# Kernel optimization log

Hardware: AMD Instinct MI355X
Metric: run time of the kernel (lower is better)

## Reference

```python
import jax, jax.numpy as jnp
import numpy as np

B, N, C, D = 2, 6, 64, 40
FH, FW = 12, 33
IMG_H, IMG_W = 384, 1056
NX, NY, NZ = 100, 100, 4
LOWER = np.array([-50.0, -50.0, -10.0], np.float32)   # xbound[0], ybound[0], zbound[0]
DXV = np.array([1.0, 1.0, 5.0], np.float32)           # voxel sizes


def _conv(x, w, pad):
    return jax.lax.conv_general_dilated(x, w, (1, 1), [(pad, pad), (pad, pad)],
                                        dimension_numbers=('NCHW', 'OIHW', 'NCHW'))


def _bn(x, s, b):
    return x * s[None, :, None, None] + b[None, :, None, None]


def _se(x, w1, b1, w2, b2):
    m = x.mean((2, 3))                                   # global avg pool -> (B, C)
    g = jax.nn.sigmoid(jax.nn.silu(m @ w1.T + b1) @ w2.T + b2)
    return x * g[:, :, None, None]


def _frustum():
    ds = jnp.arange(4.0, 44.0, 1.0)                      # (D,) depth bins
    xs = jnp.linspace(0.0, IMG_W - 1.0, FW)
    ys = jnp.linspace(0.0, IMG_H - 1.0, FH)
    f = jnp.stack(jnp.broadcast_arrays(xs[None, None, :], ys[None, :, None], ds[:, None, None]), -1)
    return f.reshape(-1, 3)                              # (D*FH*FW, 3) in (x_px, y_px, depth)


def reference(feats, rots, trans, intrinsics, nw1, bn1s, bn1b, se1w1, se1b1, se1w2, se1b2,
              nw2, bn2s, bn2b, dhw, dhb, chw, chb, bcw1, bcs1, bcb1, bcsw1, bcsb1, bcsw2,
              bcsb2, bcw2, bcs2, bcb2, dw1, ds1, db1, dw2, db2):
    BN = B * N
    # ---- CamEncoderV2 neck + heads (backbone 1280ch@1/32 features given directly) ----
    x = jax.nn.silu(_bn(_conv(feats, nw1, 0), bn1s, bn1b))
    x = _se(x, se1w1, se1b1, se1w2, se1b2)
    x = jax.nn.silu(_bn(_conv(x, nw2, 1), bn2s, bn2b))
    depth = jax.nn.softmax(_conv(x, dhw, 0) + dhb[None, :, None, None], axis=1)  # (BN, D, FH, FW)
    ctx = _conv(x, chw, 0) + chb[None, :, None, None]                            # (BN, C, FH, FW)
    # ---- geometry: pixel frustum -> ego-frame points ----
    rots_f = rots.reshape(BN, 3, 3)
    trans_f = trans.reshape(BN, 3)
    K = intrinsics.reshape(BN, 3, 3)
    pts = _frustum()                                     # (P0, 3), P0 = D*FH*FW
    d = pts[:, 2]
    fx, fy = K[:, 0, 0][:, None], K[:, 1, 1][:, None]
    cx, cy = K[:, 0, 2][:, None], K[:, 1, 2][:, None]
    cam = jnp.stack([(pts[None, :, 0] - cx) * d[None, :] / fx,
                     (pts[None, :, 1] - cy) * d[None, :] / fy,
                     jnp.broadcast_to(d[None, :], (BN, d.shape[0]))], -1)        # (BN, P0, 3)
    geom = jnp.einsum('bij,bpj->bpi', rots_f, cam) + trans_f[:, None, :]
    geom = geom.reshape(B, -1, 3)                        # (B, N*P0, 3)
    # ---- lift: outer product context x depth ----
    ff = (ctx[:, None, :, :, :] * depth[:, :, None, :, :])                       # (BN, D, C, FH, FW)
    ff = ff.transpose(0, 1, 3, 4, 2).reshape(B, -1, C)                           # (B, N*P0, C)
    # ---- splat: voxel pooling (scatter-add into BEV grid) ----
    idx = jnp.floor((geom - jnp.asarray(LOWER)) / jnp.asarray(DXV)).astype(jnp.int32)
    valid = jnp.all((idx >= 0) & (idx < jnp.array([NX, NY, NZ])), axis=-1)
    sid = idx[..., 2] * (NX * NY) + idx[..., 0] * NY + idx[..., 1]
    sid = jnp.where(valid, sid, 0)
    ffm = ff * valid[..., None]
    pooled = jax.vmap(lambda f, i: jax.ops.segment_sum(f, i, num_segments=NZ * NX * NY))(ffm, sid)
    bev = pooled.reshape(B, NZ, NX, NY, C).transpose(0, 1, 4, 2, 3).reshape(B, NZ * C, NX, NY)
    # ---- BEVCompressorV2 (residual conv-SE-conv) ----
    h = jax.nn.relu(_bn(_conv(bev, bcw1, 1), bcs1, bcb1))
    h = _se(h, bcsw1, bcsb1, bcsw2, bcsb2)
    h = jax.nn.relu(_bn(_conv(h, bcw2, 1), bcs2, bcb2))
    bev = bev + h
    # ---- decoder ----
    h = jax.nn.relu(_bn(_conv(bev, dw1, 1), ds1, db1))
    out = _conv(h, dw2, 0) + db2[None, :, None, None]    # (B, nz*num_classes, NX, NY)
    return out.reshape(B, 4, NZ, NX, NY)


def setup_inputs():
    f32 = jnp.float32
    ks = jax.random.split(jax.random.key(0), 16)
    feats = jax.random.normal(ks[0], (B * N, 1280, FH, FW), f32) * 0.5
    # cam->ego: z_cam -> x_ego, -x_cam -> y_ego, -y_cam -> z_ego, plus per-camera yaw
    Rbase = np.array([[0., 0., 1.], [-1., 0., 0.], [0., -1., 0.]], np.float32)
    yaw = np.deg2rad(np.arange(N) * 60.0).astype(np.float32)
    c, s = np.cos(yaw), np.sin(yaw)
    Rz = np.zeros((N, 3, 3), np.float32)
    Rz[:, 0, 0] = c; Rz[:, 0, 1] = -s; Rz[:, 1, 0] = s; Rz[:, 1, 1] = c; Rz[:, 2, 2] = 1.0
    rots = jnp.asarray(np.broadcast_to(np.einsum('nij,jk->nik', Rz, Rbase), (B, N, 3, 3)).copy())
    trans = jax.random.normal(ks[1], (B, N, 3), f32) * 1.0
    K = np.array([[800., 0., 528.], [0., 800., 192.], [0., 0., 1.]], np.float32)
    intrinsics = jnp.asarray(np.broadcast_to(K, (B, N, 3, 3)).copy())

    def w(k, shape, fan_in):
        return jax.random.normal(k, shape, f32) * np.float32(np.sqrt(2.0 / fan_in))

    kk = jax.random.split(ks[2], 16)
    return dict(
        feats=feats, rots=rots, trans=trans, intrinsics=intrinsics,
        nw1=w(kk[0], (256, 1280, 1, 1), 1280), bn1s=jnp.ones(256, f32), bn1b=jnp.zeros(256, f32),
        se1w1=w(kk[1], (32, 256), 256), se1b1=jnp.zeros(32, f32),
        se1w2=w(kk[2], (256, 32), 32), se1b2=jnp.zeros(256, f32),
        nw2=w(kk[3], (256, 256, 3, 3), 2304), bn2s=jnp.ones(256, f32), bn2b=jnp.zeros(256, f32),
        dhw=w(kk[4], (40, 256, 1, 1), 256), dhb=jnp.zeros(40, f32),
        chw=w(kk[5], (64, 256, 1, 1), 256), chb=jnp.zeros(64, f32),
        bcw1=w(kk[6], (256, 256, 3, 3), 2304), bcs1=jnp.ones(256, f32), bcb1=jnp.zeros(256, f32),
        bcsw1=w(kk[7], (16, 256), 256), bcsb1=jnp.zeros(16, f32),
        bcsw2=w(kk[8], (256, 16), 16), bcsb2=jnp.zeros(256, f32),
        bcw2=w(kk[9], (256, 256, 3, 3), 2304), bcs2=jnp.ones(256, f32), bcb2=jnp.zeros(256, f32),
        dw1=w(kk[10], (128, 256, 3, 3), 2304), ds1=jnp.ones(128, f32), db1=jnp.zeros(128, f32),
        dw2=w(kk[11], (16, 128, 1, 1), 128), db2=jnp.zeros(16, f32),
    )
```

## Files before the change

### kernel.cpp

```cpp
#include <hip/hip_runtime.h>
#include <hip/hip_bf16.h>
#include <cmath>


typedef __attribute__((ext_vector_type(8))) short short8;
typedef __attribute__((ext_vector_type(4))) float floatx4;
typedef __hip_bfloat16 hb;

__device__ __forceinline__ float sigf(float x){ return 1.0f/(1.0f+expf(-x)); }
__device__ __forceinline__ float siluf(float x){ return x*sigf(x); }
__device__ __forceinline__ void split2(float v, hb* h, hb* l){
  hb hv = __float2bfloat16(v);
  *h = hv; *l = __float2bfloat16(v - __bfloat162float(hv));
}

__global__ __launch_bounds__(256) void k_trans_featsP(
    const float* __restrict__ feats, hb* __restrict__ Fph, hb* __restrict__ Fpl)
{
  __shared__ float tile[64][65];
  int n = blockIdx.z;
  int p0 = blockIdx.x*64;
  int c0 = blockIdx.y*64;
  int tid = threadIdx.x;
  int tr = tid >> 6;
  int tc = tid & 63;
  #pragma unroll
  for (int it=0; it<16; ++it){
    int ci = c0 + it*4 + tr;
    int p = p0 + tc;
    float v = 0.f;
    if (p < 396) v = feats[((size_t)n*1280 + ci)*396 + p];
    tile[it*4+tr][tc] = v;
  }
  __syncthreads();
  #pragma unroll
  for (int iter=0; iter<2; ++iter){
    int idx = iter*256 + tid;
    int oc = idx >> 6;
    int pl = idx & 63;
    int p = p0 + pl;
    if (p < 396){
      int P = n*396 + p;
      int T = P >> 4, mm = P & 15;
      int kb = (c0 >> 5) + (oc >> 2);
      int q = oc & 3;
      int lane = q*16 + mm;
      size_t o = (((size_t)T*40 + kb)*64 + lane)*8;
      #pragma unroll
      for (int j=0; j<8; ++j){
        hb hv, lv; split2(tile[oc*8+j][pl], &hv, &lv);
        Fph[o+j] = hv; Fpl[o+j] = lv;
      }
    }
  }
}

__global__ __launch_bounds__(256) void k_wpack1(
    const float* __restrict__ W, hb* __restrict__ Wph, hb* __restrict__ Wpl)
{
  int i = blockIdx.x*256 + threadIdx.x;
  if (i >= 40*16*512) return;
  int j = i & 7;
  int lane = (i>>3) & 63;
  int t2 = i >> 9;
  int nb = t2 & 15;
  int kb = t2 >> 4;
  int ci = kb*32 + (lane>>4)*8 + j;
  int co = nb*16 + (lane&15);
  hb hv, lv; split2(W[(size_t)co*1280 + ci], &hv, &lv);
  Wph[i] = hv; Wpl[i] = lv;
}

__global__ __launch_bounds__(256) void k_wpack(
    const float* __restrict__ W, hb* __restrict__ Wph, hb* __restrict__ Wpl, int NB)
{
  int i = blockIdx.x*256 + threadIdx.x;
  int total = 9*8*NB*512;
  if (i >= total) return;
  int j = i & 7;
  int t1 = i >> 3;
  int lane = t1 & 63;
  int t2 = t1 >> 6;
  int nb = t2 % NB;
  int t3 = t2 / NB;
  int kb = t3 & 7;
  int tap = t3 >> 3;
  int ci = kb*32 + (lane>>4)*8 + j;
  int co = nb*16 + (lane&15);
  hb hv, lv; split2(W[(size_t)co*2304 + ci*9 + tap], &hv, &lv);
  Wph[i] = hv; Wpl[i] = lv;
}

__global__ __launch_bounds__(256) void k_wpackT(
    const float* __restrict__ W, hb* __restrict__ Wph, hb* __restrict__ Wpl, int NB)
{
  int i = blockIdx.x*256 + threadIdx.x;
  int total = 9*8*NB*512;
  if (i >= total) return;
  int j = i & 7;
  int t1 = i >> 3;
  int lane = t1 & 63;
  int t2 = t1 >> 6;
  int nb = t2 % NB;
  int t3 = t2 / NB;
  int tap = t3 % 9;
  int kb = t3 / 9;
  int ci = kb*32 + (lane>>4)*8 + j;
  int co = nb*16 + (lane&15);
  hb hv, lv; split2(W[(size_t)co*2304 + ci*9 + tap], &hv, &lv);
  Wph[i] = hv; Wpl[i] = lv;
}

__global__ __launch_bounds__(256) void k_wpackH(
    const float* __restrict__ dhw, const float* __restrict__ chw,
    hb* __restrict__ Wph, hb* __restrict__ Wpl)
{
  int i = blockIdx.x*256 + threadIdx.x;
  if (i >= 8*7*512) return;
  int j = i & 7;
  int t1 = i >> 3;
  int lane = t1 & 63;
  int t2 = t1 >> 6;
  int nb = t2 % 7;
  int kb = t2 / 7;
  int ci = kb*32 + (lane>>4)*8 + j;
  int co = nb*16 + (lane&15);
  float w = 0.f;
  if (co < 40) w = dhw[(size_t)co*256 + ci];
  else if (co < 104) w = chw[(size_t)(co-40)*256 + ci];
  hb hv, lv; split2(w, &hv, &lv);
  Wph[i] = hv; Wpl[i] = lv;
}

__global__ __launch_bounds__(256) void k_mfma_gemm1(
    const hb* __restrict__ Fph, const hb* __restrict__ Fpl,
    const hb* __restrict__ Wph, const hb* __restrict__ Wpl,
    const float* __restrict__ bns, const float* __restrict__ bnb,
    float* __restrict__ out)
{
  __shared__ short8 lbh[256], lbl[256];
  int tid = threadIdx.x;
  int wv = tid >> 6, lane = tid & 63;
  int cog = blockIdx.y;
  int Pbase = blockIdx.x*128 + wv*32;
  int q = lane >> 4;
  int T0 = blockIdx.x*8 + wv*2; if (T0 > 296) T0 = 296;
  int T1 = T0 + 1;              if (T1 > 296) T1 = 296;
  size_t a0 = (size_t)T0*2560 + lane;
  size_t a1 = (size_t)T1*2560 + lane;
  const short8* gAh = (const short8*)(const void*)Fph;
  const short8* gAl = (const short8*)(const void*)Fpl;
  const short8* gWh = (const short8*)(const void*)Wph;
  const short8* gWl = (const short8*)(const void*)Wpl;
  size_t sb = (size_t)(cog*4 + wv)*64 + lane;
  floatx4 acc[2][4];
  #pragma unroll
  for (int i=0;i<2;++i)
    #pragma unroll
    for (int j=0;j<4;++j) acc[i][j] = (floatx4)(0.f);
  short8 ph = gWh[sb], pw = gWl[sb];
  short8 cah0 = gAh[a0], cal0 = gAl[a0], cah1 = gAh[a1], cal1 = gAl[a1];
  for (int kb=0; kb<40; ++kb){
    __syncthreads();
    lbh[tid] = ph; lbl[tid] = pw;
    int nx = (kb+1 < 40) ? kb+1 : 39;
    ph = gWh[(size_t)nx*1024 + sb]; pw = gWl[(size_t)nx*1024 + sb];
    __syncthreads();
    short8 nah0 = gAh[a0 + (size_t)nx*64];
    short8 nal0 = gAl[a0 + (size_t)nx*64];
    short8 nah1 = gAh[a1 + (size_t)nx*64];
    short8 nal1 = gAl[a1 + (size_t)nx*64];
    #pragma unroll
    for (int nb=0; nb<4; ++nb){
      short8 bh = lbh[nb*64 + lane];
      short8 bl = lbl[nb*64 + lane];
      acc[0][nb] = __builtin_amdgcn_mfma_f32_16x16x32_bf16(cah0, bh, acc[0][nb], 0,0,0);
      acc[0][nb] = __builtin_amdgcn_mfma_f32_16x16x32_bf16(cah0, bl, acc[0][nb], 0,0,0);
      acc[0][nb] = __builtin_amdgcn_mfma_f32_16x16x32_bf16(cal0, bh, acc[0][nb], 0,0,0);
      acc[1][nb] = __builtin_amdgcn_mfma_f32_16x16x32_bf16(cah1, bh, acc[1][nb], 0,0,0);
      acc[1][nb] = __builtin_amdgcn_mfma_f32_16x16x32_bf16(cah1, bl, acc[1][nb], 0,0,0);
      acc[1][nb] = __builtin_amdgcn_mfma_f32_16x16x32_bf16(cal1, bh, acc[1][nb], 0,0,0);
    }
    cah0 = nah0; cal0 = nal0; cah1 = nah1; cal1 = nal1;
  }
  int n16 = lane & 15;
  #pragma unroll
  for (int mg=0; mg<2; ++mg){
    #pragma unroll
    for (int nb=0; nb<4; ++nb){
      int co = cog*64 + nb*16 + n16;
      float s = bns[co], bv = bnb[co];
      #pragma unroll
      for (int r=0; r<4; ++r){
        int P = Pbase + mg*16 + q*4 + r;
        if (P < 4752) out[(size_t)P*256 + co] = siluf(acc[mg][nb][r]*s + bv);
      }
    }
  }
}

__global__ __launch_bounds__(256) void k_meanN(
    const float* __restrict__ x1, float* __restrict__ mean)
{
  int n = blockIdx.x; int c = threadIdx.x;
  float s = 0.f;
  for (int p=0; p<396; ++p) s += x1[((size_t)n*396+p)*256 + c];
  mean[n*256+c] = s*(1.f/396.f);
}

__global__ __launch_bounds__(256) void k_se_fc(
    const float* __restrict__ mean, const float* __restrict__ w1, const float* __restrict__ b1,
    const float* __restrict__ w2, const float* __restrict__ b2, float* __restrict__ g,
    int H, float inv)
{
  __shared__ float m[256];
  __shared__ float h[32];
  int n = blockIdx.x; int t = threadIdx.x;
  m[t] = mean[n*256 + t] * inv;
  __syncthreads();
  if (t < H){
    float s = b1[t];
    for (int c=0; c<256; ++c) s += m[c]*w1[t*256+c];
    h[t] = siluf(s);
  }
  __syncthreads();
  float s = b2[t];
  for (int j=0; j<H; ++j) s += h[j]*w2[t*H+j];
  g[n*256+t] = sigf(s);
}

__global__ __launch_bounds__(256) void k_topad(
    const float* __restrict__ x1, const float* __restrict__ g,
    hb* __restrict__ Xh, hb* __restrict__ Xl)
{
  int y = blockIdx.x;
  int n = blockIdx.y;
  int c = threadIdx.x;
  float gc = g[n*256+c];
  for (int xx=0; xx<35; ++xx){
    float v = 0.f;
    if (y>=1 && y<=12 && xx>=1 && xx<=33)
      v = x1[((size_t)n*396 + (y-1)*33 + (xx-1))*256 + c]*gc;
    hb hv, lv; split2(v, &hv, &lv);
    size_t o = (((size_t)n*14+y)*35+xx)*256 + c;
    Xh[o] = hv; Xl[o] = lv;
  }
}

__global__ __launch_bounds__(256) void k_conv3s_mfma(
    const hb* __restrict__ Xh, const hb* __restrict__ Xl,
    const hb* __restrict__ Wph, const hb* __restrict__ Wpl,
    const float* __restrict__ bns, const float* __restrict__ bnb,
    hb* __restrict__ outh, hb* __restrict__ outl)
{
  __shared__ short8 lbh[256], lbl[256];
  int tid = threadIdx.x;
  int wv = tid >> 6, lane = tid & 63;
  int cog = blockIdx.y;
  int Pbase = blockIdx.x*128 + wv*32;
  int m = lane & 15, q = lane >> 4;
  int P0 = Pbase + m;      if (P0 > 4751) P0 = 4751;
  int P1 = Pbase + 16 + m; if (P1 > 4751) P1 = 4751;
  int n0 = P0/396, pim0 = P0%396;
  int n1 = P1/396, pim1 = P1%396;
  size_t base0 = (size_t)((n0*14 + pim0/33)*35 + pim0%33)*32 + q;
  size_t base1 = (size_t)((n1*14 + pim1/33)*35 + pim1%33)*32 + q;
  const short8* gAh = (const short8*)(const void*)Xh;
  const short8* gAl = (const short8*)(const void*)Xl;
  const short8* gWh = (const short8*)(const void*)Wph;
  const short8* gWl = (const short8*)(const void*)Wpl;
  size_t sb = (size_t)(cog*4 + wv)*64 + lane;
  floatx4 acc[2][4];
  #pragma unroll
  for (int i=0;i<2;++i)
    #pragma unroll
    for (int j=0;j<4;++j) acc[i][j] = (floatx4)(0.f);
  short8 ph = gWh[sb], pw = gWl[sb];
  short8 cah0 = gAh[base0], cal0 = gAl[base0], cah1 = gAh[base1], cal1 = gAl[base1];
  for (int idx=0; idx<72; ++idx){
    __syncthreads();
    lbh[tid] = ph; lbl[tid] = pw;
    int nx = (idx+1 < 72) ? idx+1 : 71;
    ph = gWh[(size_t)nx*1024 + sb]; pw = gWl[(size_t)nx*1024 + sb];
    __syncthreads();
    int tap = nx >> 3, kb = nx & 7;
    int dy = (tap*11) >> 5;
    int dx = tap - dy*3;
    int ao = (dy*35+dx)*32 + kb*4;
    short8 nah0 = gAh[base0 + ao];
    short8 nal0 = gAl[base0 + ao];
    short8 nah1 = gAh[base1 + ao];
    short8 nal1 = gAl[base1 + ao];
    #pragma unroll
    for (int nb=0; nb<4; ++nb){
      short8 bh = lbh[nb*64 + lane];
      short8 bl = lbl[nb*64 + lane];
      acc[0][nb] = __builtin_amdgcn_mfma_f32_16x16x32_bf16(cah0, bh, acc[0][nb], 0,0,0);
      acc[0][nb] = __builtin_amdgcn_mfma_f32_16x16x32_bf16(cah0, bl, acc[0][nb], 0,0,0);
      acc[0][nb] = __builtin_amdgcn_mfma_f32_16x16x32_bf16(cal0, bh, acc[0][nb], 0,0,0);
      acc[1][nb] = __builtin_amdgcn_mfma_f32_16x16x32_bf16(cah1, bh, acc[1][nb], 0,0,0);
      acc[1][nb] = __builtin_amdgcn_mfma_f32_16x16x32_bf16(cah1, bl, acc[1][nb], 0,0,0);
      acc[1][nb] = __builtin_amdgcn_mfma_f32_16x16x32_bf16(cal1, bh, acc[1][nb], 0,0,0);
    }
    cah0 = nah0; cal0 = nal0; cah1 = nah1; cal1 = nal1;
  }
  int n16 = lane & 15;
  #pragma unroll
  for (int mg=0; mg<2; ++mg){
    #pragma unroll
    for (int r=0; r<4; ++r){
      int P = Pbase + mg*16 + q*4 + r;
      if (P < 4752){
        #pragma unroll
        for (int nb=0; nb<4; ++nb){
          int co = cog*64 + nb*16 + n16;
          float v = siluf(acc[mg][nb][r]*bns[co] + bnb[co]);
          hb hv, lv; split2(v, &hv, &lv);
          outh[(size_t)P*256 + co] = hv;
          outl[(size_t)P*256 + co] = lv;
        }
      }
    }
  }
}

__global__ __launch_bounds__(256) void k_headsM(
    const hb* __restrict__ x2h, const hb* __restrict__ x2l,
    const hb* __restrict__ Whh, const hb* __restrict__ Whl,
    const float* __restrict__ dhb, const float* __restrict__ chb,
    float* __restrict__ dep, float* __restrict__ ctx2)
{
  __shared__ short8 lbh[256], lbl[256];
  int tid = threadIdx.x;
  int wv = tid >> 6, lane = tid & 63;
  int cog = blockIdx.y;
  int nb0 = cog*4;
  int nbN = cog ? 3 : 4;
  int Pbase = blockIdx.x*128 + wv*32;
  int m = lane & 15, q = lane >> 4;
  int P0 = Pbase + m;      if (P0 > 4751) P0 = 4751;
  int P1 = Pbase + 16 + m; if (P1 > 4751) P1 = 4751;
  size_t rA0 = (size_t)P0*32 + q;
  size_t rA1 = (size_t)P1*32 + q;
  const short8* gAh = (const short8*)(const void*)x2h;
  const short8* gAl = (const short8*)(const void*)x2l;
  const short8* gWh = (const short8*)(const void*)Whh;
  const short8* gWl = (const short8*)(const void*)Whl;
  floatx4 acc[2][4];
  #pragma unroll
  for (int i=0;i<2;++i)
    #pragma unroll
    for (int j=0;j<4;++j) acc[i][j] = (floatx4)(0.f);
  for (int kb=0; kb<8; ++kb){
    __syncthreads();
    for (int i=tid; i<nbN*64; i+=256){
      lbh[i] = gWh[(size_t)(kb*7 + nb0)*64 + i];
      lbl[i] = gWl[(size_t)(kb*7 + nb0)*64 + i];
    }
    __syncthreads();
    short8 ah0 = gAh[rA0 + kb*4], al0 = gAl[rA0 + kb*4];
    short8 ah1 = gAh[rA1 + kb*4], al1 = gAl[rA1 + kb*4];
    for (int nb=0; nb<nbN; ++nb){
      short8 bh = lbh[nb*64 + lane];
      short8 bl = lbl[nb*64 + lane];
      acc[0][nb] = __builtin_amdgcn_mfma_f32_16x16x32_bf16(ah0, bh, acc[0][nb], 0,0,0);
      acc[0][nb] = __builtin_amdgcn_mfma_f32_16x16x32_bf16(ah0, bl, acc[0][nb], 0,0,0);
      acc[0][nb] = __builtin_amdgcn_mfma_f32_16x16x32_bf16(al0, bh, acc[0][nb], 0,0,0);
      acc[1][nb] = __builtin_amdgcn_mfma_f32_16x16x32_bf16(ah1, bh, acc[1][nb], 0,0,0);
      acc[1][nb] = __builtin_amdgcn_mfma_f32_16x16x32_bf16(ah1, bl, acc[1][nb], 0,0,0);
      acc[1][nb] = __builtin_amdgcn_mfma_f32_16x16x32_bf16(al1, bh, acc[1][nb], 0,0,0);
    }
  }
  int n16 = lane & 15;
  #pragma unroll
  for (int mg=0; mg<2; ++mg){
    #pragma unroll
    for (int r=0; r<4; ++r){
      int P = Pbase + mg*16 + q*4 + r;
      if (P < 4752){
        int nn = P/396, pim = P%396;
        for (int nb=0; nb<nbN; ++nb){
          int co = cog*64 + nb*16 + n16;
          float v = acc[mg][nb][r];
          if (co < 40)
            dep[((size_t)nn*40 + co)*396 + pim] = v + dhb[co];
          else if (co < 104)
            ctx2[((size_t)nn*396 + pim)*64 + (co-40)] = v + chb[co-40];
        }
      }
    }
  }
}

__global__ __launch_bounds__(256) void k_softmax40(float* __restrict__ dep)
{
  int i = blockIdx.x*256 + threadIdx.x;
  if (i >= 12*396) return;
  int n = i/396, p = i%396;
  float* base = dep + (size_t)n*40*396 + p;
  float mx = -1e30f;
  for (int d=0; d<40; ++d) mx = fmaxf(mx, base[(size_t)d*396]);
  float s = 0.f;
  for (int d=0; d<40; ++d){ float e = expf(base[(size_t)d*396]-mx); base[(size_t)d*396]=e; s+=e; }
  float inv = 1.f/s;
  for (int d=0; d<40; ++d) base[(size_t)d*396] *= inv;
}

__global__ __launch_bounds__(256) void k_geom(
    const float* __restrict__ rots, const float* __restrict__ trans,
    const float* __restrict__ intr, int* __restrict__ vox, int* __restrict__ cnt)
{
  int pt = blockIdx.x*256 + threadIdx.x;
  if (pt >= 190080) return;
  int b = pt/95040; int r = pt%95040;
  int n = r/15840;  int r2 = r%15840;
  int d = r2/396;   int pim = r2%396;
  int y = pim/33, x = pim%33;
  int bn = b*6+n;
  const float* R = rots + (size_t)bn*9;
  const float* T = trans + (size_t)bn*3;
  const float* K = intr + (size_t)bn*9;
  float fx=K[0], cx=K[2], fy=K[4], cy=K[5];
  float xs = (float)x * 32.96875f;
  float ys = (float)((double)y * (383.0/11.0));
  float dv = 4.0f + (float)d;
  float camx = (xs-cx)*dv/fx;
  float camy = (ys-cy)*dv/fy;
  float gx = R[0]*camx + R[1]*camy + R[2]*dv + T[0];
  float gy = R[3]*camx + R[4]*camy + R[5]*dv + T[1];
  float gz = R[6]*camx + R[7]*camy + R[8]*dv + T[2];
  int ix = (int)floorf(gx + 50.f);
  int iy = (int)floorf(gy + 50.f);
  int iz = (int)floorf((gz + 10.f)/5.f);
  bool valid = (ix>=0 && ix<100 && iy>=0 && iy<100 && iz>=0 && iz<4);
  int sid = iz*10000 + ix*100 + iy;
  vox[pt] = valid ? sid : -1;
  if (valid) atomicAdd(&cnt[b*40000 + sid], 1);
}

__global__ __launch_bounds__(256) void k_scan1(
    const int* __restrict__ cnt, int* __restrict__ off, int* __restrict__ bsum)
{
  __shared__ int s[256];
  int t = threadIdx.x;
  int i = blockIdx.x*256 + t;
  int v = (i < 80000) ? cnt[i] : 0;
  s[t] = v; __syncthreads();
  for (int o=1;o<256;o<<=1){
    int x = (t>=o) ? s[t-o] : 0;
    __syncthreads();
    s[t] += x;
    __syncthreads();
  }
  if (i < 80000) off[i] = s[t] - v;
  if (t == 255) bsum[blockIdx.x] = s[255];
}

__global__ void k_scan2(int* __restrict__ bsum, int nblk)
{
  if (threadIdx.x==0 && blockIdx.x==0){
    int run = 0;
    for (int j=0;j<nblk;++j){ int t = bsum[j]; bsum[j] = run; run += t; }
  }
}

__global__ __launch_bounds__(256) void k_scan3(
    int* __restrict__ off, const int* __restrict__ bsum, int* __restrict__ cur)
{
  int i = blockIdx.x*256 + threadIdx.x;
  if (i >= 80000) return;
  int o = off[i] + bsum[i>>8];
  off[i] = o;
  cur[i] = o;
}

__global__ __launch_bounds__(256) void k_fill(
    const int* __restrict__ vox, int* __restrict__ cur, int* __restrict__ list)
{
  int pt = blockIdx.x*256 + threadIdx.x;
  if (pt >= 190080) return;
  int s = vox[pt];
  if (s < 0) return;
  int b = pt/95040;
  int slot = atomicAdd(&cur[b*40000 + s], 1);
  list[slot] = pt;
}

__global__ __launch_bounds__(256) void k_gather(
    const int* __restrict__ off, const int* __restrict__ cnt, const int* __restrict__ list,
    const float* __restrict__ ctx2, const float* __restrict__ dep, float* __restrict__ bev)
{
  int tid = threadIdx.x;
  int bv = blockIdx.x*4 + (tid>>6);
  int c = tid & 63;
  int b = bv/40000, sid = bv%40000;
  int st = off[bv], nn = cnt[bv];
  float s = 0.f;
  for (int k=0;k<nn;++k){
    int pt = list[st+k];
    int r = pt%95040;
    int bn = b*6 + r/15840;
    int r2 = r%15840;
    int dd = r2/396, pim = r2%396;
    s += ctx2[((size_t)bn*396+pim)*64 + c] * dep[((size_t)bn*40+dd)*396 + pim];
  }
  int iz = sid/10000, rem = sid%10000;
  bev[(size_t)b*2560000 + (size_t)iz*640000 + (size_t)c*10000 + rem] = s;
}

__global__ __launch_bounds__(256) void k_tohwc2(
    const float* __restrict__ in, hb* __restrict__ Ah, hb* __restrict__ Al,
    const float* __restrict__ g)
{
  __shared__ float tile[32*105];
  int py = blockIdx.x;
  int b  = blockIdx.y;
  int cg = blockIdx.z;
  int tid = threadIdx.x;
  bool inner = (py >= 1 && py <= 100);
  if (inner){
    if (tid < 64){ int cil = tid & 31; int col = (tid>>5) ? 101 : 0; tile[cil*105 + col] = 0.f; }
    for (int i = tid; i < 3200; i += 256){
      int cil = i / 100, x = i % 100;
      int ci = cg*32 + cil;
      tile[cil*105 + (x+1)] = in[(((size_t)b*256 + ci)*100 + (py-1))*100 + x];
    }
  }
  __syncthreads();
  for (int i = tid; i < 32*102; i += 256){
    int px = i >> 5, cil = i & 31;
    int ci = cg*32 + cil;
    float v = 0.f;
    if (inner){
      v = tile[cil*105 + px];
      if (g) v *= g[b*256 + ci];
    }
    hb hv, lv; split2(v, &hv, &lv);
    size_t o = (((size_t)b*102 + py)*102 + px)*256 + ci;
    Ah[o] = hv; Al[o] = lv;
  }
}

__global__ __launch_bounds__(256) void k_rowmean(
    const float* __restrict__ in, float* __restrict__ out, int rowlen, float inv)
{
  __shared__ float ws[4];
  int row = blockIdx.x; int t = threadIdx.x;
  const float* p = in + (size_t)row*rowlen;
  float s = 0.f;
  for (int i=t; i<rowlen; i+=256) s += p[i];
  #pragma unroll
  for (int off=32; off; off>>=1) s += __shfl_down(s, off);
  if ((t&63)==0) ws[t>>6] = s;
  __syncthreads();
  if (t==0) out[row] = (ws[0]+ws[1]+ws[2]+ws[3]) * inv;
}

__global__ __launch_bounds__(256) void k_conv3_bevm(
    const hb* __restrict__ Ah, const hb* __restrict__ Al,
    const hb* __restrict__ Wph, const hb* __restrict__ Wpl,
    const float* __restrict__ bns, const float* __restrict__ bnb,
    const float* __restrict__ res, float* __restrict__ out, int Cout, int NBG)
{
  __shared__ __align__(16) short sAh[10*18*44];
  __shared__ __align__(16) short sAl[10*18*44];
  __shared__ short8 lbh[2][256], lbl[2][256];
  const int NB = Cout >> 4;
  int tid = threadIdx.x;
  int wv = tid >> 6, lane = tid & 63;
  int L = blockIdx.x;
  int spatial = L / (NBG*2);
  int rem = L % (NBG*2);
  int cog = rem % NBG;
  int bb  = rem / NBG;
  int xg = spatial % 7, yg = spatial / 7;
  int x0 = xg*16;
  int y0 = yg*8 + wv;
  int m = lane & 15, q = lane >> 4;
  int nb0 = cog*4;
  floatx4 acc[2][4];
  #pragma unroll
  for (int i=0;i<2;++i)
    #pragma unroll
    for (int j=0;j<4;++j) acc[i][j] = (floatx4)(0.f);

  const short8* gAh = (const short8*)(const void*)Ah;
  const short8* gAl = (const short8*)(const void*)Al;
  const short8* gWh = (const short8*)(const void*)Wph;
  const short8* gWl = (const short8*)(const void*)Wpl;
  const size_t nbstride = (size_t)NB*64;
  const size_t sb = (size_t)(nb0 + wv)*64 + lane;

  short8 ph = gWh[sb], pl = gWl[sb];
  int cur = 0;

  for (int kb=0; kb<8; ++kb){
    #pragma unroll 3
    for (int tap=0; tap<9; ++tap){
      int idx2 = kb*9 + tap;
      if (tap == 0){
        __syncthreads();
        for (int i = tid; i < 720; i += 256){
          int rc = i >> 2, part = i & 3;
          int r = rc / 18, c = rc % 18;
          int yr = yg*8 + r; if (yr > 101) yr = 101;
          int xc = x0 + c;   if (xc > 101) xc = 101;
          size_t so = ((size_t)((bb*102 + yr)*102 + xc))*32 + kb*4 + part;
          short8 vh = gAh[so], vl = gAl[so];
          int dst = (r*18 + c)*44 + part*8;
          *(short8*)(sAh + dst) = vh;
          *(short8*)(sAl + dst) = vl;
        }
      }
      lbh[cur][tid] = ph; lbl[cur][tid] = pl;
      int nx = (idx2+1 < 72) ? idx2+1 : 71;
      ph = gWh[(size_t)nx*nbstride + sb];
      pl = gWl[(size_t)nx*nbstride + sb];
      __syncthreads();
      int dy = (tap*11) >> 5;
      int dx = tap - dy*3;
      int cc = dx + m;
      int a0 = ((wv + dy)*18 + cc)*44 + q*8;
      int a1 = ((wv + 4 + dy)*18 + cc)*44 + q*8;
      short8 cah0 = *(const short8*)(sAh + a0);
      short8 cal0 = *(const short8*)(sAl + a0);
      short8 cah1 = *(const short8*)(sAh + a1);
      short8 cal1 = *(const short8*)(sAl + a1);
      #pragma unroll
      for (int nb=0; nb<4; ++nb){
        short8 bh = lbh[cur][nb*64 + lane];
        short8 bl = lbl[cur][nb*64 + lane];
        acc[0][nb] = __builtin_amdgcn_mfma_f32_16x16x32_bf16(cah0, bh, acc[0][nb], 0,0,0);
        acc[0][nb] = __builtin_amdgcn_mfma_f32_16x16x32_bf16(cah0, bl, acc[0][nb], 0,0,0);
        acc[0][nb] = __builtin_amdgcn_mfma_f32_16x16x32_bf16(cal0, bh, acc[0][nb], 0,0,0);
        acc[1][nb] = __builtin_amdgcn_mfma_f32_16x16x32_bf16(cah1, bh, acc[1][nb], 0,0,0);
        acc[1][nb] = __builtin_amdgcn_mfma_f32_16x16x32_bf16(cah1, bl, acc[1][nb], 0,0,0);
        acc[1][nb] = __builtin_amdgcn_mfma_f32_16x16x32_bf16(cal1, bh, acc[1][nb], 0,0,0);
      }
      cur ^= 1;
    }
  }

  int n = lane & 15;
  int xq = x0 + q*4;
  #pragma unroll
  for (int mg=0; mg<2; ++mg){
    int yo = y0 + mg*4;
    if (yo < 100 && xq < 100){
      #pragma unroll
      for (int nb=0; nb<4; ++nb){
        int co = cog*64 + nb*16 + n;
        float s = bns[co], bv = bnb[co];
        floatx4 a = acc[mg][nb];
        float4 v;
        v.x = fmaxf(a[0]*s+bv, 0.f);
        v.y = fmaxf(a[1]*s+bv, 0.f);
        v.z = fmaxf(a[2]*s+bv, 0.f);
        v.w = fmaxf(a[3]*s+bv, 0.f);
        size_t o = ((size_t)(bb*Cout+co)*100 + yo)*100 + xq;
        if (res){
          float4 rv = *(const float4*)(res + o);
          v.x += rv.x; v.y += rv.y; v.z += rv.z; v.w += rv.w;
        }
        *(float4*)(out + o) = v;
      }
    }
  }
}

__global__ __launch_bounds__(256) void k_final2(
    const float* __restrict__ h, const float* __restrict__ W, const float* __restrict__ bias,
    float* __restrict__ out)
{
  __shared__ float wsl[2048];
  __shared__ float bs[16];
  int tid = threadIdx.x;
  int b = blockIdx.y;
  for (int i=tid; i<2048; i+=256) wsl[i] = W[i];
  if (tid < 16) bs[tid] = bias[tid];
  __syncthreads();
  int pix = blockIdx.x*256 + tid;
  if (pix >= 10000) return;
  float acc[16];
  #pragma unroll
  for (int oc=0; oc<16; ++oc) acc[oc] = bs[oc];
  const float* hb_ = h + (size_t)b*128*10000 + pix;
  for (int ci=0; ci<128; ++ci){
    float hv = hb_[(size_t)ci*10000];
    #pragma unroll
    for (int oc=0; oc<16; ++oc) acc[oc] += hv * wsl[oc*128 + ci];
  }
  #pragma unroll
  for (int oc=0; oc<16; ++oc)
    out[((size_t)(b*16+oc))*10000 + pix] = acc[oc];
}

extern "C" void kernel_launch(void* const* d_in, const int* in_sizes, int n_in,
                              void* d_out, int out_size, void* d_ws, size_t ws_size,
                              hipStream_t stream)
{
  (void)in_sizes; (void)n_in; (void)out_size; (void)ws_size;
  const float* feats = (const float*)d_in[0];
  const float* rots  = (const float*)d_in[1];
  const float* trans = (const float*)d_in[2];
  const float* intr  = (const float*)d_in[3];
  const float* nw1   = (const float*)d_in[4];
  const float* bn1s  = (const float*)d_in[5];
  const float* bn1b  = (const float*)d_in[6];
  const float* se1w1 = (const float*)d_in[7];
  const float* se1b1 = (const float*)d_in[8];
  const float* se1w2 = (const float*)d_in[9];
  const float* se1b2 = (const float*)d_in[10];
  const float* nw2   = (const float*)d_in[11];
  const float* bn2s  = (const float*)d_in[12];
  const float* bn2b  = (const float*)d_in[13];
  const float* dhw   = (const float*)d_in[14];
  const float* dhb   = (const float*)d_in[15];
  const float* chw   = (const float*)d_in[16];
  const float* chb   = (const float*)d_in[17];
  const float* bcw1  = (const float*)d_in[18];
  const float* bcs1  = (const float*)d_in[19];
  const float* bcb1  = (const float*)d_in[20];
  const float* bcsw1 = (const float*)d_in[21];
  const float* bcsb1 = (const float*)d_in[22];
  const float* bcsw2 = (const float*)d_in[23];
  const float* bcsb2 = (const float*)d_in[24];
  const float* bcw2  = (const float*)d_in[25];
  const float* bcs2  = (const float*)d_in[26];
  const float* bcb2  = (const float*)d_in[27];
  const float* dw1   = (const float*)d_in[28];
  const float* ds1   = (const float*)d_in[29];
  const float* db1   = (const float*)d_in[30];
  const float* dw2   = (const float*)d_in[31];
  const float* db2   = (const float*)d_in[32];
  float* out = (float*)d_out;

  float* ws = (float*)d_ws;
  float* bev   = ws;
  float* h1    = ws + 5120000;
  hb*    Ah    = (hb*)(ws + 10240000);
  hb*    Al    = (hb*)(ws + 12903424);
  float* x2    = ws + 15566848;
  float* S5    = ws + 16783360;
  float* dep   = ws + 17373184;
  float* ctx2  = ws + 17563264;
  float* mean1 = ws + 17867392;
  float* g1    = mean1 + 3072;
  float* mean2 = g1 + 3072;
  float* g2    = mean2 + 512;
  int*   vox   = (int*)(ws + 17875584);
  hb* Fph  = (hb*)bev;
  hb* Wc1h = (hb*)(bev + 3041280);
  hb* Wc1l = (hb*)(bev + 3205120);
  float* x1 = h1;
  hb* Fpl  = (hb*)(h1 + 1216512);
  hb* Xh   = (hb*)Ah;
  hb* Xl   = (hb*)Al;
  hb* Wc2h = (hb*)S5;
  hb* Wc2l = (hb*)(S5 + 294912);
  hb* x2h  = (hb*)x2;
  hb* x2l  = (hb*)(x2 + 608256);
  hb* Whh  = (hb*)S5;
  hb* Whl  = (hb*)(S5 + 14336);
  int* cnt  = (int*)h1;
  int* off  = cnt + 80000;
  int* cur  = off + 80000;
  int* bsum = cur + 80000;
  int* list = bsum + 1024;
  float* h3 = h1;
  hb* Wp1h = (hb*)x2;
  hb* Wp1l = (hb*)(x2 + 294912);
  hb* Wp3h = (hb*)(x2 + 589824);
  hb* Wp3l = (hb*)(x2 + 589824 + 147456);
  hb* Wp2h = (hb*)S5;
  hb* Wp2l = (hb*)(S5 + 294912);

  k_trans_featsP<<<dim3(7,20,12),256,0,stream>>>(feats,Fph,Fpl);
  k_wpack1<<<1280,256,0,stream>>>(nw1,Wc1h,Wc1l);
  k_mfma_gemm1<<<dim3(38,4),256,0,stream>>>(Fph,Fpl,Wc1h,Wc1l,bn1s,bn1b,x1);
  k_meanN<<<12,256,0,stream>>>(x1,mean1);
  k_se_fc<<<12,256,0,stream>>>(mean1,se1w1,se1b1,se1w2,se1b2,g1,32,1.f);
  k_topad<<<dim3(14,12),256,0,stream>>>(x1,g1,Xh,Xl);
  k_wpack<<<2304,256,0,stream>>>(nw2,Wc2h,Wc2l,16);
  k_conv3s_mfma<<<dim3(38,4),256,0,stream>>>(Xh,Xl,Wc2h,Wc2l,bn2s,bn2b,x2h,x2l);
  k_wpackH<<<112,256,0,stream>>>(dhw,chw,Whh,Whl);
  k_headsM<<<dim3(38,2),256,0,stream>>>(x2h,x2l,Whh,Whl,dhb,chb,dep,ctx2);
  k_softmax40<<<19,256,0,stream>>>(dep);

  k_wpackT<<<2304,256,0,stream>>>(bcw1,Wp1h,Wp1l,16);
  k_wpackT<<<2304,256,0,stream>>>(bcw2,Wp2h,Wp2l,16);
  k_wpackT<<<1152,256,0,stream>>>(dw1,Wp3h,Wp3l,8);

  hipMemsetAsync(cnt, 0, 80000*sizeof(int), stream);
  k_geom<<<(190080+255)/256,256,0,stream>>>(rots,trans,intr,vox,cnt);
  k_scan1<<<313,256,0,stream>>>(cnt,off,bsum);
  k_scan2<<<1,64,0,stream>>>(bsum,313);
  k_scan3<<<(80000+255)/256,256,0,stream>>>(off,bsum,cur);
  k_fill<<<(190080+255)/256,256,0,stream>>>(vox,cur,list);
  k_gather<<<20000,256,0,stream>>>(off,cnt,list,ctx2,dep,bev);

  k_tohwc2<<<dim3(102,2,8),256,0,stream>>>(bev,Ah,Al,nullptr);
  k_conv3_bevm<<<728,256,0,stream>>>(Ah,Al,Wp1h,Wp1l,bcs1,bcb1,nullptr,h1,256,4);
  k_rowmean<<<512,256,0,stream>>>(h1,mean2,10000,1e-4f);
  k_se_fc<<<2,256,0,stream>>>(mean2,bcsw1,bcsb1,bcsw2,bcsb2,g2,16,1.f);
  k_tohwc2<<<dim3(102,2,8),256,0,stream>>>(h1,Ah,Al,g2);
  k_conv3_bevm<<<728,256,0,stream>>>(Ah,Al,Wp2h,Wp2l,bcs2,bcb2,bev,bev,256,4);
  k_tohwc2<<<dim3(102,2,8),256,0,stream>>>(bev,Ah,Al,nullptr);
  k_conv3_bevm<<<364,256,0,stream>>>(Ah,Al,Wp3h,Wp3l,ds1,db1,nullptr,h3,128,2);
  k_final2<<<dim3(40,2),256,0,stream>>>(h3,dw2,db2,out);
}
```

Before: 687.0 us.

## Merge weight-pack and SE kernels, tile image conv in LDS, fuse BEV repack into gather

Several weight-packing launches are merged into two kernels, and the mean and SE-FC steps are fused into one kernel. The image 3x3 conv is rewritten to stage a spatial input tile in LDS per channel block and reuse it across the nine taps, with double-buffered weight fragments. The BEV gather now writes the padded bf16 hi/lo HWC layout directly, and a small kernel zeros the padding ring, so the first k_tohwc2 pass is dropped. Together these cut launch count and redundant global traffic, at the cost of more LDS use and a more complex conv indexing scheme.

```diff
diff --git a/kernel.cpp b/kernel.cpp
--- a/kernel.cpp
+++ b/kernel.cpp
@@ -55,48 +55,53 @@
   }
 }
 
-__global__ __launch_bounds__(256) void k_wpack1(
-    const float* __restrict__ W, hb* __restrict__ Wph, hb* __restrict__ Wpl)
+__global__ __launch_bounds__(256) void k_wpackE(
+    const float* __restrict__ nw1, const float* __restrict__ nw2,
+    hb* __restrict__ Wc1h, hb* __restrict__ Wc1l,
+    hb* __restrict__ Wc2h, hb* __restrict__ Wc2l)
 {
   int i = blockIdx.x*256 + threadIdx.x;
-  if (i >= 40*16*512) return;
-  int j = i & 7;
-  int lane = (i>>3) & 63;
-  int t2 = i >> 9;
-  int nb = t2 & 15;
-  int kb = t2 >> 4;
-  int ci = kb*32 + (lane>>4)*8 + j;
-  int co = nb*16 + (lane&15);
-  hb hv, lv; split2(W[(size_t)co*1280 + ci], &hv, &lv);
-  Wph[i] = hv; Wpl[i] = lv;
-}
-
-__global__ __launch_bounds__(256) void k_wpack(
-    const float* __restrict__ W, hb* __restrict__ Wph, hb* __restrict__ Wpl, int NB)
-{
-  int i = blockIdx.x*256 + threadIdx.x;
-  int total = 9*8*NB*512;
-  if (i >= total) return;
-  int j = i & 7;
-  int t1 = i >> 3;
-  int lane = t1 & 63;
-  int t2 = t1 >> 6;
-  int nb = t2 % NB;
-  int t3 = t2 / NB;
-  int kb = t3 & 7;
-  int tap = t3 >> 3;
-  int ci = kb*32 + (lane>>4)*8 + j;
-  int co = nb*16 + (lane&15);
-  hb hv, lv; split2(W[(size_t)co*2304 + ci*9 + tap], &hv, &lv);
-  Wph[i] = hv; Wpl[i] = lv;
-}
-
-__global__ __launch_bounds__(256) void k_wpackT(
-    const float* __restrict__ W, hb* __restrict__ Wph, hb* __restrict__ Wpl, int NB)
-{
-  int i = blockIdx.x*256 + threadIdx.x;
-  int total = 9*8*NB*512;
-  if (i >= total) return;
+  if (i < 327680){
+    int j = i & 7;
+    int lane = (i>>3) & 63;
+    int t2 = i >> 9;
+    int nb = t2 & 15;
+    int kb = t2 >> 4;
+    int ci = kb*32 + (lane>>4)*8 + j;
+    int co = nb*16 + (lane&15);
+    hb hv, lv; split2(nw1[(size_t)co*1280 + ci], &hv, &lv);
+    Wc1h[i] = hv; Wc1l[i] = lv;
+  } else {
+    int i2 = i - 327680;
+    if (i2 >= 589824) return;
+    int j = i2 & 7;
+    int t1 = i2 >> 3;
+    int lane = t1 & 63;
+    int t2 = t1 >> 6;
+    int nb = t2 % 16;
+    int t3 = t2 / 16;
+    int tap = t3 % 9;
+    int kb = t3 / 9;
+    int ci = kb*32 + (lane>>4)*8 + j;
+    int co = nb*16 + (lane&15);
+    hb hv, lv; split2(nw2[(size_t)co*2304 + ci*9 + tap], &hv, &lv);
+    Wc2h[i2] = hv; Wc2l[i2] = lv;
+  }
+}
+
+__global__ __launch_bounds__(256) void k_wpackT3(
+    const float* __restrict__ bcw1, const float* __restrict__ bcw2,
+    const float* __restrict__ dw1,
+    hb* __restrict__ W1h, hb* __restrict__ W1l,
+    hb* __restrict__ W2h, hb* __restrict__ W2l,
+    hb* __restrict__ W3h, hb* __restrict__ W3l)
+{
+  int gi = blockIdx.x*256 + threadIdx.x;
+  const float* W; hb* Wh; hb* Wl; int NB; int i;
+  if (gi < 589824){ W = bcw1; Wh = W1h; Wl = W1l; NB = 16; i = gi; }
+  else if (gi < 1179648){ W = bcw2; Wh = W2h; Wl = W2l; NB = 16; i = gi - 589824; }
+  else if (gi < 1474560){ W = dw1; Wh = W3h; Wl = W3l; NB = 8; i = gi - 1179648; }
+  else return;
   int j = i & 7;
   int t1 = i >> 3;
   int lane = t1 & 63;
@@ -108,7 +113,7 @@
   int ci = kb*32 + (lane>>4)*8 + j;
   int co = nb*16 + (lane&15);
   hb hv, lv; split2(W[(size_t)co*2304 + ci*9 + tap], &hv, &lv);
-  Wph[i] = hv; Wpl[i] = lv;
+  Wh[i] = hv; Wl[i] = lv;
 }
 
 __global__ __launch_bounds__(256) void k_wpackH(
@@ -199,24 +204,36 @@
   }
 }
 
-__global__ __launch_bounds__(256) void k_meanN(
-    const float* __restrict__ x1, float* __restrict__ mean)
-{
-  int n = blockIdx.x; int c = threadIdx.x;
-  float s = 0.f;
-  for (int p=0; p<396; ++p) s += x1[((size_t)n*396+p)*256 + c];
-  mean[n*256+c] = s*(1.f/396.f);
-}
-
-__global__ __launch_bounds__(256) void k_se_fc(
-    const float* __restrict__ mean, const float* __restrict__ w1, const float* __restrict__ b1,
-    const float* __restrict__ w2, const float* __restrict__ b2, float* __restrict__ g,
-    int H, float inv)
+__global__ __launch_bounds__(256) void k_meanse(
+    const float* __restrict__ x1, const float* __restrict__ w1, const float* __restrict__ b1,
+    const float* __restrict__ w2, const float* __restrict__ b2, float* __restrict__ g)
 {
   __shared__ float m[256];
   __shared__ float h[32];
   int n = blockIdx.x; int t = threadIdx.x;
-  m[t] = mean[n*256 + t] * inv;
+  float s = 0.f;
+  for (int p=0; p<396; ++p) s += x1[((size_t)n*396+p)*256 + t];
+  m[t] = s*(1.f/396.f);
+  __syncthreads();
+  if (t < 32){
+    float s2 = b1[t];
+    for (int c=0; c<256; ++c) s2 += m[c]*w1[t*256+c];
+    h[t] = siluf(s2);
+  }
+  __syncthreads();
+  float s3 = b2[t];
+  for (int j=0; j<32; ++j) s3 += h[j]*w2[t*32+j];
+  g[n*256+t] = sigf(s3);
+}
+
+__global__ __launch_bounds__(256) void k_se_fc(
+    const float* __restrict__ mean, const float* __restrict__ w1, const float* __restrict__ b1,
+    const float* __restrict__ w2, const float* __restrict__ b2, float* __restrict__ g, int H)
+{
+  __shared__ float m[256];
+  __shared__ float h[32];
+  int n = blockIdx.x; int t = threadIdx.x;
+  m[t] = mean[n*256 + t];
   __syncthreads();
   if (t < H){
     float s = b1[t];
@@ -247,77 +264,104 @@
   }
 }
 
-__global__ __launch_bounds__(256) void k_conv3s_mfma(
+__global__ __launch_bounds__(256) void k_conv3_img(
     const hb* __restrict__ Xh, const hb* __restrict__ Xl,
     const hb* __restrict__ Wph, const hb* __restrict__ Wpl,
     const float* __restrict__ bns, const float* __restrict__ bnb,
     hb* __restrict__ outh, hb* __restrict__ outl)
 {
-  __shared__ short8 lbh[256], lbl[256];
+  __shared__ __align__(16) short sAh[10*18*44];
+  __shared__ __align__(16) short sAl[10*18*44];
+  __shared__ short8 lbh[2][256], lbl[2][256];
   int tid = threadIdx.x;
   int wv = tid >> 6, lane = tid & 63;
-  int cog = blockIdx.y;
-  int Pbase = blockIdx.x*128 + wv*32;
+  int xg = blockIdx.x;
+  int n = blockIdx.y >> 1, yg = blockIdx.y & 1;
+  int cog = blockIdx.z;
+  int x0 = xg*16;
+  int y0 = yg*8 + wv;
   int m = lane & 15, q = lane >> 4;
-  int P0 = Pbase + m;      if (P0 > 4751) P0 = 4751;
-  int P1 = Pbase + 16 + m; if (P1 > 4751) P1 = 4751;
-  int n0 = P0/396, pim0 = P0%396;
-  int n1 = P1/396, pim1 = P1%396;
-  size_t base0 = (size_t)((n0*14 + pim0/33)*35 + pim0%33)*32 + q;
-  size_t base1 = (size_t)((n1*14 + pim1/33)*35 + pim1%33)*32 + q;
+  floatx4 acc[2][4];
+  #pragma unroll
+  for (int i=0;i<2;++i)
+    #pragma unroll
+    for (int j=0;j<4;++j) acc[i][j] = (floatx4)(0.f);
+
   const short8* gAh = (const short8*)(const void*)Xh;
   const short8* gAl = (const short8*)(const void*)Xl;
   const short8* gWh = (const short8*)(const void*)Wph;
   const short8* gWl = (const short8*)(const void*)Wpl;
-  size_t sb = (size_t)(cog*4 + wv)*64 + lane;
-  floatx4 acc[2][4];
-  #pragma unroll
-  for (int i=0;i<2;++i)
-    #pragma unroll
-    for (int j=0;j<4;++j) acc[i][j] = (floatx4)(0.f);
-  short8 ph = gWh[sb], pw = gWl[sb];
-  short8 cah0 = gAh[base0], cal0 = gAl[base0], cah1 = gAh[base1], cal1 = gAl[base1];
-  for (int idx=0; idx<72; ++idx){
-    __syncthreads();
-    lbh[tid] = ph; lbl[tid] = pw;
-    int nx = (idx+1 < 72) ? idx+1 : 71;
-    ph = gWh[(size_t)nx*1024 + sb]; pw = gWl[(size_t)nx*1024 + sb];
-    __syncthreads();
-    int tap = nx >> 3, kb = nx & 7;
-    int dy = (tap*11) >> 5;
-    int dx = tap - dy*3;
-    int ao = (dy*35+dx)*32 + kb*4;
-    short8 nah0 = gAh[base0 + ao];
-    short8 nal0 = gAl[base0 + ao];
-    short8 nah1 = gAh[base1 + ao];
-    short8 nal1 = gAl[base1 + ao];
-    #pragma unroll
-    for (int nb=0; nb<4; ++nb){
-      short8 bh = lbh[nb*64 + lane];
-      short8 bl = lbl[nb*64 + lane];
-      acc[0][nb] = __builtin_amdgcn_mfma_f32_16x16x32_bf16(cah0, bh, acc[0][nb], 0,0,0);
-      acc[0][nb] = __builtin_amdgcn_mfma_f32_16x16x32_bf16(cah0, bl, acc[0][nb], 0,0,0);
-      acc[0][nb] = __builtin_amdgcn_mfma_f32_16x16x32_bf16(cal0, bh, acc[0][nb], 0,0,0);
-      acc[1][nb] = __builtin_amdgcn_mfma_f32_16x16x32_bf16(cah1, bh, acc[1][nb], 0,0,0);
-      acc[1][nb] = __builtin_amdgcn_mfma_f32_16x16x32_bf16(cah1, bl, acc[1][nb], 0,0,0);
-      acc[1][nb] = __builtin_amdgcn_mfma_f32_16x16x32_bf16(cal1, bh, acc[1][nb], 0,0,0);
-    }
-    cah0 = nah0; cal0 = nal0; cah1 = nah1; cal1 = nal1;
-  }
+  const size_t sb = (size_t)(cog*4 + wv)*64 + lane;
+  const size_t nbase = (size_t)n*14*35*32;
+
+  short8 ph = gWh[sb], pl = gWl[sb];
+  int cur = 0;
+
+  for (int kb=0; kb<8; ++kb){
+    #pragma unroll 3
+    for (int tap=0; tap<9; ++tap){
+      int idx2 = kb*9 + tap;
+      if (tap == 0){
+        __syncthreads();
+        for (int i = tid; i < 720; i += 256){
+          int rc = i >> 2, part = i & 3;
+          int r = rc / 18, c2 = rc % 18;
+          int yr = yg*8 + r; if (yr > 13) yr = 13;
+          int xc = x0 + c2;  if (xc > 34) xc = 34;
+          size_t so = nbase + (size_t)(yr*35 + xc)*32 + kb*4 + part;
+          short8 vh = gAh[so], vl = gAl[so];
+          int dst = (r*18 + c2)*44 + part*8;
+          *(short8*)(sAh + dst) = vh;
+          *(short8*)(sAl + dst) = vl;
+        }
+      }
+      lbh[cur][tid] = ph; lbl[cur][tid] = pl;
+      int nx = (idx2+1 < 72) ? idx2+1 : 71;
+      ph = gWh[(size_t)nx*1024 + sb];
+      pl = gWl[(size_t)nx*1024 + sb];
+      __syncthreads();
+      int dy = (tap*11) >> 5;
+      int dx = tap - dy*3;
+      int cc = dx + m;
+      int a0 = ((wv + dy)*18 + cc)*44 + q*8;
+      int a1 = ((wv + 4 + dy)*18 + cc)*44 + q*8;
+      short8 cah0 = *(const short8*)(sAh + a0);
+      short8 cal0 = *(const short8*)(sAl + a0);
+      short8 cah1 = *(const short8*)(sAh + a1);
+      short8 cal1 = *(const short8*)(sAl + a1);
+      #pragma unroll
+      for (int nb=0; nb<4; ++nb){
+        short8 bh = lbh[cur][nb*64 + lane];
+        short8 bl = lbl[cur][nb*64 + lane];
+        acc[0][nb] = __builtin_amdgcn_mfma_f32_16x16x32_bf16(cah0, bh, acc[0][nb], 0,0,0);
+        acc[0][nb] = __builtin_amdgcn_mfma_f32_16x16x32_bf16(cah0, bl, acc[0][nb], 0,0,0);
+        acc[0][nb] = __builtin_amdgcn_mfma_f32_16x16x32_bf16(cal0, bh, acc[0][nb], 0,0,0);
+        acc[1][nb] = __builtin_amdgcn_mfma_f32_16x16x32_bf16(cah1, bh, acc[1][nb], 0,0,0);
+        acc[1][nb] = __builtin_amdgcn_mfma_f32_16x16x32_bf16(cah1, bl, acc[1][nb], 0,0,0);
+        acc[1][nb] = __builtin_amdgcn_mfma_f32_16x16x32_bf16(cal1, bh, acc[1][nb], 0,0,0);
+      }
+      cur ^= 1;
+    }
+  }
+
   int n16 = lane & 15;
   #pragma unroll
   for (int mg=0; mg<2; ++mg){
-    #pragma unroll
-    for (int r=0; r<4; ++r){
-      int P = Pbase + mg*16 + q*4 + r;
-      if (P < 4752){
-        #pragma unroll
-        for (int nb=0; nb<4; ++nb){
-          int co = cog*64 + nb*16 + n16;
-          float v = siluf(acc[mg][nb][r]*bns[co] + bnb[co]);
-          hb hv, lv; split2(v, &hv, &lv);
-          outh[(size_t)P*256 + co] = hv;
-          outl[(size_t)P*256 + co] = lv;
+    int oy = y0 + mg*4;
+    if (oy < 12){
+      #pragma unroll
+      for (int r=0; r<4; ++r){
+        int ox = x0 + q*4 + r;
+        if (ox < 33){
+          int P = n*396 + oy*33 + ox;
+          #pragma unroll
+          for (int nb=0; nb<4; ++nb){
+            int co = cog*64 + nb*16 + n16;
+            float v = siluf(acc[mg][nb][r]*bns[co] + bnb[co]);
+            hb hv, lv; split2(v, &hv, &lv);
+            outh[(size_t)P*256 + co] = hv;
+            outl[(size_t)P*256 + co] = lv;
+          }
         }
       }
     }
@@ -486,9 +530,28 @@
   list[slot] = pt;
 }
 
+__global__ __launch_bounds__(256) void k_zero_ring(hb* __restrict__ Ah, hb* __restrict__ Al)
+{
+  int i = blockIdx.x*256 + threadIdx.x;
+  if (i >= 2*404*256) return;
+  int c = i & 255;
+  int t = i >> 8;
+  int b = t / 404;
+  int ridx = t % 404;
+  int py, px;
+  if (ridx < 102){ py = 0; px = ridx; }
+  else if (ridx < 204){ py = 101; px = ridx-102; }
+  else if (ridx < 304){ py = ridx-204+1; px = 0; }
+  else { py = ridx-304+1; px = 101; }
+  size_t o = (((size_t)b*102 + py)*102 + px)*256 + c;
+  hb z = __float2bfloat16(0.f);
+  Ah[o] = z; Al[o] = z;
+}
+
 __global__ __launch_bounds__(256) void k_gather(
     const int* __restrict__ off, const int* __restrict__ cnt, const int* __restrict__ list,
-    const float* __restrict__ ctx2, const float* __restrict__ dep, float* __restrict__ bev)
+    const float* __restrict__ ctx2, const float* __restrict__ dep, float* __restrict__ bev,
+    hb* __restrict__ Ah, hb* __restrict__ Al)
 {
   int tid = threadIdx.x;
   int bv = blockIdx.x*4 + (tid>>6);
@@ -506,6 +569,10 @@
   }
   int iz = sid/10000, rem = sid%10000;
   bev[(size_t)b*2560000 + (size_t)iz*640000 + (size_t)c*10000 + rem] = s;
+  int ix = rem/100, iy = rem%100;
+  size_t oh = (((size_t)b*102 + (ix+1))*102 + (iy+1))*256 + iz*64 + c;
+  hb hv, lv; split2(s, &hv, &lv);
+  Ah[oh] = hv; Al[oh] = lv;
 }
 
 __global__ __launch_bounds__(256) void k_tohwc2(
@@ -776,20 +843,16 @@
   hb* Wp2l = (hb*)(S5 + 294912);
 
   k_trans_featsP<<<dim3(7,20,12),256,0,stream>>>(feats,Fph,Fpl);
-  k_wpack1<<<1280,256,0,stream>>>(nw1,Wc1h,Wc1l);
+  k_wpackE<<<3584,256,0,stream>>>(nw1,nw2,Wc1h,Wc1l,Wc2h,Wc2l);
   k_mfma_gemm1<<<dim3(38,4),256,0,stream>>>(Fph,Fpl,Wc1h,Wc1l,bn1s,bn1b,x1);
-  k_meanN<<<12,256,0,stream>>>(x1,mean1);
-  k_se_fc<<<12,256,0,stream>>>(mean1,se1w1,se1b1,se1w2,se1b2,g1,32,1.f);
+  k_meanse<<<12,256,0,stream>>>(x1,se1w1,se1b1,se1w2,se1b2,g1);
   k_topad<<<dim3(14,12),256,0,stream>>>(x1,g1,Xh,Xl);
-  k_wpack<<<2304,256,0,stream>>>(nw2,Wc2h,Wc2l,16);
-  k_conv3s_mfma<<<dim3(38,4),256,0,stream>>>(Xh,Xl,Wc2h,Wc2l,bn2s,bn2b,x2h,x2l);
+  k_conv3_img<<<dim3(3,24,4),256,0,stream>>>(Xh,Xl,Wc2h,Wc2l,bn2s,bn2b,x2h,x2l);
   k_wpackH<<<112,256,0,stream>>>(dhw,chw,Whh,Whl);
   k_headsM<<<dim3(38,2),256,0,stream>>>(x2h,x2l,Whh,Whl,dhb,chb,dep,ctx2);
   k_softmax40<<<19,256,0,stream>>>(dep);
 
-  k_wpackT<<<2304,256,0,stream>>>(bcw1,Wp1h,Wp1l,16);
-  k_wpackT<<<2304,256,0,stream>>>(bcw2,Wp2h,Wp2l,16);
-  k_wpackT<<<1152,256,0,stream>>>(dw1,Wp3h,Wp3l,8);
+  k_wpackT3<<<5760,256,0,stream>>>(bcw1,bcw2,dw1,Wp1h,Wp1l,Wp2h,Wp2l,Wp3h,Wp3l);
 
   hipMemsetAsync(cnt, 0, 80000*sizeof(int), stream);
   k_geom<<<(190080+255)/256,256,0,stream>>>(rots,trans,intr,vox,cnt);
@@ -797,12 +860,12 @@
   k_scan2<<<1,64,0,stream>>>(bsum,313);
   k_scan3<<<(80000+255)/256,256,0,stream>>>(off,bsum,cur);
   k_fill<<<(190080+255)/256,256,0,stream>>>(vox,cur,list);
-  k_gather<<<20000,256,0,stream>>>(off,cnt,list,ctx2,dep,bev);
-
-  k_tohwc2<<<dim3(102,2,8),256,0,stream>>>(bev,Ah,Al,nullptr);
+  k_zero_ring<<<808,256,0,stream>>>(Ah,Al);
+  k_gather<<<20000,256,0,stream>>>(off,cnt,list,ctx2,dep,bev,Ah,Al);
+
   k_conv3_bevm<<<728,256,0,stream>>>(Ah,Al,Wp1h,Wp1l,bcs1,bcb1,nullptr,h1,256,4);
   k_rowmean<<<512,256,0,stream>>>(h1,mean2,10000,1e-4f);
-  k_se_fc<<<2,256,0,stream>>>(mean2,bcsw1,bcsb1,bcsw2,bcsb2,g2,16,1.f);
+  k_se_fc<<<2,256,0,stream>>>(mean2,bcsw1,bcsb1,bcsw2,bcsb2,g2,16);
   k_tohwc2<<<dim3(102,2,8),256,0,stream>>>(h1,Ah,Al,g2);
   k_conv3_bevm<<<728,256,0,stream>>>(Ah,Al,Wp2h,Wp2l,bcs2,bcb2,bev,bev,256,4);
   k_tohwc2<<<dim3(102,2,8),256,0,stream>>>(bev,Ah,Al,nullptr);
```

Result: faster. 671.5 us (-2.3%).
